# Performance work log

Measured on AMD Instinct MI355X. Metric: run time of the kernel, lower is better.

The kernel has to match this reference:

```python
import jax, jax.numpy as jnp
import numpy as np

B, N, P, C, H = 8, 512, 16, 512, 8
HD = C // H  # 64


def setup_inputs() -> dict:
    key = jax.random.key(0)
    k1, k2, k3, k4, k5 = jax.random.split(key, 5)
    x = jax.random.normal(k1, (B, N, P, C), dtype=jnp.float32)
    # binary observation mask; force slot 0 valid so masked mean never divides by 0
    mask = (jax.random.uniform(k2, (B, N, P)) > 0.3).astype(jnp.float32)
    mask = mask.at[:, :, 0].set(1.0)
    lens = jax.random.randint(k3, (B,), 1, N)
    lens_mask = jnp.ones((B, N), dtype=jnp.float32)
    # parameters (torch Linear stored as [in, out] here; qkv_bias=False, proj has bias)
    Wqkv = jax.random.normal(k4, (C, 3 * C), dtype=jnp.float32) * (1.0 / np.sqrt(C))
    Wproj = jax.random.normal(k5, (C, C), dtype=jnp.float32) * (1.0 / np.sqrt(C))
    bproj = jnp.zeros((C,), dtype=jnp.float32)
    return {"x": x, "mask": mask, "lens": lens, "lens_mask": lens_mask,
            "Wqkv": Wqkv, "Wproj": Wproj, "bproj": bproj}


def reference(x, mask, lens, lens_mask, Wqkv, Wproj, bproj):
    # lens / lens_mask are unused by the original forward
    b, n, p, c = x.shape
    h, hd = H, c // H
    qkv = jnp.einsum('bnpc,cd->bnpd', x, Wqkv).reshape(b, n, p, 3, h, hd)
    # q: take P-slot 0                       -> [B,H,N,hd]
    q = qkv[:, :, 0, 0].transpose(0, 2, 1, 3)
    # k: masked mean over P                  -> [B,H,N,hd]
    m = mask[..., None, None]                      # [B,N,P,1,1]
    k = (jnp.where(m > 0, qkv[:, :, :, 1], 0.0).sum(axis=2) / m.sum(axis=2))
    k = k.transpose(0, 2, 1, 3)
    # v: pack P into channel dim             -> [B,H,N,hd*P]
    v = qkv[:, :, :, 2].transpose(0, 3, 1, 4, 2).reshape(b, h, n, hd * p)
    # SDPA over N (scale by 1/sqrt(head_dim of q))
    scale = 1.0 / np.sqrt(hd)
    attn = jax.nn.softmax(jnp.einsum('bhnd,bhmd->bhnm', q, k) * scale, axis=-1)
    out = jnp.einsum('bhnm,bhme->bhne', attn, v)            # [B,H,N,hd*P]
    # unpack P back out                       -> [B,N,P,C]
    out = out.reshape(b, h, n, hd, p).transpose(0, 2, 4, 1, 3).reshape(b, n, p, c)
    return out @ Wproj + bproj
```

## Files before the change

### kernel.cpp

```cpp
#include <hip/hip_runtime.h>

typedef _Float16 f16;
typedef __attribute__((ext_vector_type(8))) _Float16 half8;
typedef __attribute__((ext_vector_type(2))) _Float16 half2v;
typedef __attribute__((ext_vector_type(4))) float float4v;

#define MODE_QK 0
#define MODE_V 1
#define MODE_PV 2
#define MODE_PROJ 3


__device__ __forceinline__ void gload16(const f16* g, f16* l) {
    __builtin_amdgcn_global_load_lds(
        (const __attribute__((address_space(1))) void*)g,
        (__attribute__((address_space(3))) void*)l, 16, 0, 0);
}

__global__ __launch_bounds__(256) void prep_kernel(
    const float* __restrict__ x, const float* __restrict__ mask,
    const float* __restrict__ Wqkv, const float* __restrict__ Wproj,
    f16* __restrict__ xf, f16* __restrict__ xmean,
    f16* __restrict__ WT, f16* __restrict__ WpT)
{
    if (blockIdx.x >= 4096) {
        int idx = (blockIdx.x - 4096) * 256 + threadIdx.x;
        if (idx < 1536 * 512) {
            int d = idx >> 9, c = idx & 511;
            WT[idx] = (f16)Wqkv[c * 1536 + d];
        } else {
            int i2 = idx - 1536 * 512;
            int d = i2 >> 9, c = i2 & 511;
            WpT[i2] = (f16)Wproj[c * 512 + d];
        }
        return;
    }
    int bn = blockIdx.x;
    int t = threadIdx.x;
    const float* xrow = x + (size_t)bn * 16 * 512;
    const float* mrow = mask + (size_t)bn * 16;
    float msum = 0.f;
    #pragma unroll
    for (int p = 0; p < 16; p++) msum += mrow[p];
    int c = t * 2;
    float a0 = 0.f, a1 = 0.f;
    #pragma unroll
    for (int p = 0; p < 16; p++) {
        float2 v = *(const float2*)(xrow + p * 512 + c);
        float m = mrow[p];
        a0 += m * v.x; a1 += m * v.y;
        half2v h; h[0] = (f16)v.x; h[1] = (f16)v.y;
        *(half2v*)(xf + (size_t)bn * 16 * 512 + p * 512 + c) = h;
    }
    float inv = 1.f / msum;
    half2v hm; hm[0] = (f16)(a0 * inv); hm[1] = (f16)(a1 * inv);
    *(half2v*)(xmean + (size_t)bn * 512 + c) = hm;
}

template<int MODE, int NXB, int NYB>
__global__ __launch_bounds__(256) void gemm128(
    const f16* __restrict__ pA, const f16* __restrict__ pA2,
    const f16* __restrict__ pB,
    f16* __restrict__ outa, f16* __restrict__ outb,
    float* __restrict__ outf, const float* __restrict__ bias)
{
    __shared__ __align__(16) f16 sm[16384];
    const int t = threadIdx.x;
    const int lane = t & 63;
    const int w = t >> 6;
    const int wm = w & 1, wn = w >> 1;
    const int quad = lane >> 4, l15 = lane & 15;

    const int chunk = (int)gridDim.x >> 3;
    const int L = ((int)blockIdx.x & 7) * chunk + ((int)blockIdx.x >> 3);
    const int xb = L & ((1 << NXB) - 1);
    const int rest = L >> NXB;
    const int yb = rest & ((1 << NYB) - 1);
    const int z = rest >> NYB;
    const int n0 = xb * 128;
    const int m0 = yb * 128;
    int vb = 0, vp = 0;

    const f16* Abase; size_t sA;
    const f16* Bbase; size_t sB;
    if constexpr (MODE == MODE_QK) {
        if (n0 < 512) { Abase = pA;  sA = 8192; }
        else          { Abase = pA2; sA = 512;  }
        Bbase = pB; sB = 512;
    } else if constexpr (MODE == MODE_V) {
        vb = z >> 4; vp = z & 15;
        Abase = pA; sA = 512;
        Bbase = pB + ((size_t)vb * 512 * 16 + vp) * 512; sB = 8192;
    } else if constexpr (MODE == MODE_PV) {
        Abase = pA + (size_t)z * 512 * 512; sA = 512;
        Bbase = pB + (size_t)z * 1024 * 512; sB = 512;
    } else {
        Abase = pA; sA = 512;
        Bbase = pB; sB = 512;
    }

    const int rlo = (lane >> 2);
    const int kof = (((lane & 3) ^ ((rlo >> 1) & 3)) * 8);
    const f16* ga0 = Abase + (size_t)(m0 + w * 16 + rlo) * sA + kof;
    const f16* ga1 = Abase + (size_t)(m0 + (w + 4) * 16 + rlo) * sA + kof;
    const f16* gb0 = Bbase + (size_t)(n0 + w * 16 + rlo) * sB + kof;
    const f16* gb1 = Bbase + (size_t)(n0 + (w + 4) * 16 + rlo) * sB + kof;

    float4v acc[4][4];
    #pragma unroll
    for (int i = 0; i < 4; i++)
        #pragma unroll
        for (int j = 0; j < 4; j++)
            acc[i][j] = (float4v){0.f, 0.f, 0.f, 0.f};

    {
        f16* d = sm;
        gload16(ga0, d + w * 512); gload16(ga1, d + (w + 4) * 512);
        gload16(gb0, d + 4096 + w * 512); gload16(gb1, d + 4096 + (w + 4) * 512);
        ga0 += 32; ga1 += 32; gb0 += 32; gb1 += 32;
    }
    const int sws = (l15 >> 1) & 3;
    int cur = 0;
    for (int kt = 0; kt < 16; kt++) {
        __syncthreads();
        if (kt < 15) {
            f16* d = sm + (cur ^ 1) * 8192;
            gload16(ga0, d + w * 512); gload16(ga1, d + (w + 4) * 512);
            gload16(gb0, d + 4096 + w * 512); gload16(gb1, d + 4096 + (w + 4) * 512);
            ga0 += 32; ga1 += 32; gb0 += 32; gb1 += 32;
        }
        const f16* Asr = sm + cur * 8192;
        const f16* Bsr = Asr + 4096;
        half8 af[4], bf[4];
        #pragma unroll
        for (int mi = 0; mi < 4; mi++)
            af[mi] = *(const half8*)&Asr[(wm * 64 + mi * 16 + l15) * 32 +
                                         ((quad ^ sws) * 8)];
        #pragma unroll
        for (int ni = 0; ni < 4; ni++)
            bf[ni] = *(const half8*)&Bsr[(wn * 64 + ni * 16 + l15) * 32 +
                                         ((quad ^ sws) * 8)];
        #pragma unroll
        for (int mi = 0; mi < 4; mi++)
            #pragma unroll
            for (int ni = 0; ni < 4; ni++)
                acc[mi][ni] = __builtin_amdgcn_mfma_f32_16x16x32_f16(
                    af[mi], bf[ni], acc[mi][ni], 0, 0, 0);
        cur ^= 1;
    }

    __syncthreads();

    if constexpr (MODE == MODE_PROJ) {
        float* pwf = (float*)sm + w * 1088;
        const int rr4 = lane >> 4, c4c = (lane & 15) * 4;
        float4v bb = *(const float4v*)&bias[n0 + wn * 64 + c4c];
        #pragma unroll
        for (int mi = 0; mi < 4; mi++) {
            #pragma unroll
            for (int ni = 0; ni < 4; ni++)
                #pragma unroll
                for (int i = 0; i < 4; i++)
                    pwf[(quad * 4 + i) * 68 + ni * 16 + l15] = acc[mi][ni][i];
            #pragma unroll
            for (int s = 0; s < 4; s++) {
                int r = s * 4 + rr4;
                float4v v = *(const float4v*)&pwf[r * 68 + c4c];
                *(float4v*)&outf[(size_t)(m0 + wm * 64 + mi * 16 + r) * 512 +
                                 n0 + wn * 64 + c4c] = v + bb;
            }
        }
    } else {
        f16* pw = sm + w * 2304;
        const int rr8 = lane >> 3, c8 = (lane & 7) * 8;
        #pragma unroll
        for (int hf = 0; hf < 2; hf++) {
            #pragma unroll
            for (int mh = 0; mh < 2; mh++) {
                int mi = hf * 2 + mh;
                #pragma unroll
                for (int ni = 0; ni < 4; ni++)
                    #pragma unroll
                    for (int i = 0; i < 4; i++)
                        pw[(mh * 16 + quad * 4 + i) * 72 + ni * 16 + l15] =
                            (f16)acc[mi][ni][i];
            }
            #pragma unroll
            for (int s = 0; s < 4; s++) {
                int r = s * 8 + rr8;
                half8 v = *(const half8*)&pw[r * 72 + c8];
                int gr = m0 + wm * 64 + hf * 32 + r;
                int gc = n0 + wn * 64 + c8;
                if constexpr (MODE == MODE_QK) {
                    int b = gr >> 9, n = gr & 511;
                    if (gc < 512)
                        *(half8*)&outa[(((size_t)(b * 8 + (gc >> 6))) * 512 + n) * 64 + (gc & 63)] = v;
                    else {
                        int jj = gc - 512;
                        *(half8*)&outb[(((size_t)(b * 8 + (jj >> 6))) * 512 + n) * 64 + (jj & 63)] = v;
                    }
                } else if constexpr (MODE == MODE_V) {
                    int h = gr >> 6, dd = gr & 63;
                    *(half8*)&outa[(((size_t)(vb * 8 + h)) * 1024 + vp * 64 + dd) * 512 + gc] = v;
                } else {
                    int p = gc >> 6, dd = gc & 63;
                    int b = z >> 3, h = z & 7;
                    *(half8*)&outa[((size_t)(b * 512 + gr) * 16 + p) * 512 + h * 64 + dd] = v;
                }
            }
        }
    }
}

__global__ __launch_bounds__(256) void qk_softmax_kernel(
    const f16* __restrict__ q, const f16* __restrict__ k, f16* __restrict__ Pout)
{
    __shared__ __align__(16) f16 sm[16896];
    const int t = threadIdx.x;
    const int lane = t & 63, w = t >> 6;
    const int quad = lane >> 4, l15 = lane & 15;
    const int L = ((int)blockIdx.x & 7) * 64 + ((int)blockIdx.x >> 3);
    const int bh = L >> 3;
    const int n0 = (L & 7) * 64;

    const f16* kbase = k + (size_t)bh * 512 * 64;
    const f16* qp = q + ((size_t)bh * 512 + n0 + w * 16 + l15) * 64 + quad * 8;
    half8 a0 = *(const half8*)qp;
    half8 a1 = *(const half8*)(qp + 32);

    float4v acc[32];
    #pragma unroll
    for (int f = 0; f < 32; f++) acc[f] = (float4v){0.f, 0.f, 0.f, 0.f};

    const int srow = lane >> 3, scol = lane & 7;
    #pragma unroll
    for (int c = 0; c < 4; c++) {
        __syncthreads();
        #pragma unroll
        for (int i = 0; i < 4; i++) {
            int ci2 = w * 4 + i;
            int row = ci2 * 8 + srow;
            gload16(kbase + c * 8192 + row * 64 + ((scol ^ (row & 7)) << 3),
                    sm + ci2 * 512 + lane * 8);
        }
        __syncthreads();
        #pragma unroll
        for (int fl = 0; fl < 8; fl++) {
            int row16 = fl * 16 + l15;
            int sw = row16 & 7;
            half8 b0 = *(const half8*)&sm[row16 * 64 + ((quad ^ sw) << 3)];
            half8 b1 = *(const half8*)&sm[row16 * 64 + (((quad + 4) ^ sw) << 3)];
            acc[c * 8 + fl] = __builtin_amdgcn_mfma_f32_16x16x32_f16(
                a0, b0, acc[c * 8 + fl], 0, 0, 0);
            acc[c * 8 + fl] = __builtin_amdgcn_mfma_f32_16x16x32_f16(
                a1, b1, acc[c * 8 + fl], 0, 0, 0);
        }
    }

    float mx0 = -3e38f, mx1 = -3e38f, mx2 = -3e38f, mx3 = -3e38f;
    #pragma unroll
    for (int f = 0; f < 32; f++) {
        mx0 = fmaxf(mx0, acc[f][0]); mx1 = fmaxf(mx1, acc[f][1]);
        mx2 = fmaxf(mx2, acc[f][2]); mx3 = fmaxf(mx3, acc[f][3]);
    }
    #pragma unroll
    for (int off = 1; off < 16; off <<= 1) {
        mx0 = fmaxf(mx0, __shfl_xor(mx0, off));
        mx1 = fmaxf(mx1, __shfl_xor(mx1, off));
        mx2 = fmaxf(mx2, __shfl_xor(mx2, off));
        mx3 = fmaxf(mx3, __shfl_xor(mx3, off));
    }
    float s0 = 0.f, s1 = 0.f, s2 = 0.f, s3 = 0.f;
    #pragma unroll
    for (int f = 0; f < 32; f++) {
        float e0 = __expf(0.125f * (acc[f][0] - mx0));
        float e1 = __expf(0.125f * (acc[f][1] - mx1));
        float e2 = __expf(0.125f * (acc[f][2] - mx2));
        float e3 = __expf(0.125f * (acc[f][3] - mx3));
        acc[f][0] = e0; acc[f][1] = e1; acc[f][2] = e2; acc[f][3] = e3;
        s0 += e0; s1 += e1; s2 += e2; s3 += e3;
    }
    #pragma unroll
    for (int off = 1; off < 16; off <<= 1) {
        s0 += __shfl_xor(s0, off);
        s1 += __shfl_xor(s1, off);
        s2 += __shfl_xor(s2, off);
        s3 += __shfl_xor(s3, off);
    }
    float r0 = 1.f / s0, r1 = 1.f / s1, r2 = 1.f / s2, r3 = 1.f / s3;

    __syncthreads();
    f16* pb = sm + w * 4224;
    const int rr = lane >> 2, cb = (lane & 3) * 64;
    #pragma unroll
    for (int cc = 0; cc < 2; cc++) {
        #pragma unroll
        for (int ff = 0; ff < 16; ff++) {
            int f = cc * 16 + ff;
            pb[(quad * 4 + 0) * 264 + ff * 16 + l15] = (f16)(acc[f][0] * r0);
            pb[(quad * 4 + 1) * 264 + ff * 16 + l15] = (f16)(acc[f][1] * r1);
            pb[(quad * 4 + 2) * 264 + ff * 16 + l15] = (f16)(acc[f][2] * r2);
            pb[(quad * 4 + 3) * 264 + ff * 16 + l15] = (f16)(acc[f][3] * r3);
        }
        size_t gb = ((size_t)bh * 512 + n0 + w * 16 + rr) * 512 + cc * 256 + cb;
        #pragma unroll
        for (int s = 0; s < 8; s++) {
            half8 v = *(const half8*)&pb[rr * 264 + cb + s * 8];
            *(half8*)&Pout[gb + s * 8] = v;
        }
    }
}

extern "C" void kernel_launch(void* const* d_in, const int* in_sizes, int n_in,
                              void* d_out, int out_size, void* d_ws, size_t ws_size,
                              hipStream_t stream)
{
    (void)in_sizes; (void)n_in; (void)out_size; (void)ws_size;
    const float* x     = (const float*)d_in[0];
    const float* mask  = (const float*)d_in[1];
    const float* Wqkv  = (const float*)d_in[4];
    const float* Wproj = (const float*)d_in[5];
    const float* bproj = (const float*)d_in[6];
    float* out = (float*)d_out;
    char* ws = (char*)d_ws;

    f16* xf16  = (f16*)(ws + 0);
    f16* vT    = (f16*)(ws + 67108864);
    f16* xmean = (f16*)(ws + 134217728);
    f16* WT    = (f16*)(ws + 138412032);
    f16* WpT   = (f16*)(ws + 139984896);
    f16* qb    = (f16*)(ws + 140509184);
    f16* kb    = (f16*)(ws + 144703488);
    f16* Pm    = (f16*)(ws + 148897792);
    f16* ypre  = xf16;

    prep_kernel<<<dim3(8192), dim3(256), 0, stream>>>(
        x, mask, Wqkv, Wproj, xf16, xmean, WT, WpT);
    gemm128<MODE_QK, 3, 5><<<dim3(256), dim3(256), 0, stream>>>(
        xf16, xmean, WT, qb, kb, nullptr, nullptr);
    gemm128<MODE_V, 2, 2><<<dim3(2048), dim3(256), 0, stream>>>(
        WT + 1024 * 512, nullptr, xf16, vT, nullptr, nullptr, nullptr);
    qk_softmax_kernel<<<dim3(512), dim3(256), 0, stream>>>(qb, kb, Pm);
    gemm128<MODE_PV, 3, 2><<<dim3(2048), dim3(256), 0, stream>>>(
        Pm, nullptr, vT, ypre, nullptr, nullptr, nullptr);
    gemm128<MODE_PROJ, 2, 9><<<dim3(2048), dim3(256), 0, stream>>>(
        ypre, nullptr, WpT, nullptr, nullptr, out, bproj);
}
```

Baseline: 421.9 us.

## Triple-buffer GEMM K-loop and load full K tile at once in QK softmax

The shared GEMM kernel moves from double to triple buffering in LDS. It uses explicit vmcnt waits and raw barriers so two tiles are in flight while one is computed, which should hide global-to-LDS latency better. The QK softmax kernel now loads the whole 512x64 K block into LDS up front, replacing four chunked load/sync rounds with a single wait. Both kernels use more LDS (48KB and 64KB), which can lower occupancy.

```diff
diff --git a/kernel.cpp b/kernel.cpp
--- a/kernel.cpp
+++ b/kernel.cpp
@@ -64,7 +64,7 @@
     f16* __restrict__ outa, f16* __restrict__ outb,
     float* __restrict__ outf, const float* __restrict__ bias)
 {
-    __shared__ __align__(16) f16 sm[16384];
+    __shared__ __align__(16) f16 sm[24576];
     const int t = threadIdx.x;
     const int lane = t & 63;
     const int w = t >> 6;
@@ -113,41 +113,62 @@
         for (int j = 0; j < 4; j++)
             acc[i][j] = (float4v){0.f, 0.f, 0.f, 0.f};
 
-    {
-        f16* d = sm;
-        gload16(ga0, d + w * 512); gload16(ga1, d + (w + 4) * 512);
-        gload16(gb0, d + 4096 + w * 512); gload16(gb1, d + 4096 + (w + 4) * 512);
-        ga0 += 32; ga1 += 32; gb0 += 32; gb1 += 32;
-    }
     const int sws = (l15 >> 1) & 3;
-    int cur = 0;
-    for (int kt = 0; kt < 16; kt++) {
-        __syncthreads();
-        if (kt < 15) {
-            f16* d = sm + (cur ^ 1) * 8192;
-            gload16(ga0, d + w * 512); gload16(ga1, d + (w + 4) * 512);
-            gload16(gb0, d + 4096 + w * 512); gload16(gb1, d + 4096 + (w + 4) * 512);
-            ga0 += 32; ga1 += 32; gb0 += 32; gb1 += 32;
-        }
-        const f16* Asr = sm + cur * 8192;
-        const f16* Bsr = Asr + 4096;
-        half8 af[4], bf[4];
-        #pragma unroll
-        for (int mi = 0; mi < 4; mi++)
-            af[mi] = *(const half8*)&Asr[(wm * 64 + mi * 16 + l15) * 32 +
-                                         ((quad ^ sws) * 8)];
-        #pragma unroll
-        for (int ni = 0; ni < 4; ni++)
-            bf[ni] = *(const half8*)&Bsr[(wn * 64 + ni * 16 + l15) * 32 +
-                                         ((quad ^ sws) * 8)];
-        #pragma unroll
-        for (int mi = 0; mi < 4; mi++)
-            #pragma unroll
-            for (int ni = 0; ni < 4; ni++)
-                acc[mi][ni] = __builtin_amdgcn_mfma_f32_16x16x32_f16(
-                    af[mi], bf[ni], acc[mi][ni], 0, 0, 0);
-        cur ^= 1;
-    }
+
+#define STAGE(dst)                                                     \
+    do {                                                               \
+        f16* d_ = (dst);                                               \
+        gload16(ga0, d_ + w * 512); gload16(ga1, d_ + (w + 4) * 512);  \
+        gload16(gb0, d_ + 4096 + w * 512);                             \
+        gload16(gb1, d_ + 4096 + (w + 4) * 512);                       \
+        ga0 += 32; ga1 += 32; gb0 += 32; gb1 += 32;                    \
+    } while (0)
+
+#define COMPUTE(buf)                                                         \
+    do {                                                                     \
+        const f16* Asr_ = (buf);                                             \
+        const f16* Bsr_ = Asr_ + 4096;                                       \
+        half8 af[4], bf[4];                                                  \
+        _Pragma("unroll")                                                    \
+        for (int mi = 0; mi < 4; mi++)                                       \
+            af[mi] = *(const half8*)&Asr_[(wm * 64 + mi * 16 + l15) * 32 +   \
+                                          ((quad ^ sws) * 8)];               \
+        _Pragma("unroll")                                                    \
+        for (int ni = 0; ni < 4; ni++)                                       \
+            bf[ni] = *(const half8*)&Bsr_[(wn * 64 + ni * 16 + l15) * 32 +   \
+                                          ((quad ^ sws) * 8)];               \
+        _Pragma("unroll")                                                    \
+        for (int mi = 0; mi < 4; mi++)                                       \
+            _Pragma("unroll")                                                \
+            for (int ni = 0; ni < 4; ni++)                                   \
+                acc[mi][ni] = __builtin_amdgcn_mfma_f32_16x16x32_f16(        \
+                    af[mi], bf[ni], acc[mi][ni], 0, 0, 0);                   \
+    } while (0)
+
+    f16* pc = sm;
+    f16* pn = sm + 8192;
+    f16* pf = sm + 16384;
+    STAGE(pc);
+    STAGE(pn);
+    for (int kt = 0; kt < 14; kt++) {
+        asm volatile("s_waitcnt vmcnt(4)" ::: "memory");
+        __builtin_amdgcn_s_barrier();
+        __builtin_amdgcn_sched_barrier(0);
+        STAGE(pf);
+        COMPUTE(pc);
+        f16* tmp = pc; pc = pn; pn = pf; pf = tmp;
+    }
+    asm volatile("s_waitcnt vmcnt(4)" ::: "memory");
+    __builtin_amdgcn_s_barrier();
+    __builtin_amdgcn_sched_barrier(0);
+    COMPUTE(pc);
+    { f16* tmp = pc; pc = pn; pn = pf; pf = tmp; }
+    asm volatile("s_waitcnt vmcnt(0)" ::: "memory");
+    __builtin_amdgcn_s_barrier();
+    __builtin_amdgcn_sched_barrier(0);
+    COMPUTE(pc);
+#undef STAGE
+#undef COMPUTE
 
     __syncthreads();
 
@@ -215,7 +236,7 @@
 __global__ __launch_bounds__(256) void qk_softmax_kernel(
     const f16* __restrict__ q, const f16* __restrict__ k, f16* __restrict__ Pout)
 {
-    __shared__ __align__(16) f16 sm[16896];
+    __shared__ __align__(16) f16 sm[32768];
     const int t = threadIdx.x;
     const int lane = t & 63, w = t >> 6;
     const int quad = lane >> 4, l15 = lane & 15;
@@ -224,37 +245,33 @@
     const int n0 = (L & 7) * 64;
 
     const f16* kbase = k + (size_t)bh * 512 * 64;
+
+    #pragma unroll
+    for (int i = 0; i < 16; i++) {
+        int cid = i * 256 + t;
+        int row = cid >> 3, off = cid & 7;
+        gload16(kbase + row * 64 + ((off ^ (row & 7)) << 3),
+                sm + i * 2048 + w * 512 + (lane & 63) * 8);
+    }
     const f16* qp = q + ((size_t)bh * 512 + n0 + w * 16 + l15) * 64 + quad * 8;
     half8 a0 = *(const half8*)qp;
     half8 a1 = *(const half8*)(qp + 32);
 
+    asm volatile("s_waitcnt vmcnt(0)" ::: "memory");
+    __builtin_amdgcn_s_barrier();
+    __builtin_amdgcn_sched_barrier(0);
+
     float4v acc[32];
     #pragma unroll
     for (int f = 0; f < 32; f++) acc[f] = (float4v){0.f, 0.f, 0.f, 0.f};
-
-    const int srow = lane >> 3, scol = lane & 7;
-    #pragma unroll
-    for (int c = 0; c < 4; c++) {
-        __syncthreads();
-        #pragma unroll
-        for (int i = 0; i < 4; i++) {
-            int ci2 = w * 4 + i;
-            int row = ci2 * 8 + srow;
-            gload16(kbase + c * 8192 + row * 64 + ((scol ^ (row & 7)) << 3),
-                    sm + ci2 * 512 + lane * 8);
-        }
-        __syncthreads();
-        #pragma unroll
-        for (int fl = 0; fl < 8; fl++) {
-            int row16 = fl * 16 + l15;
-            int sw = row16 & 7;
-            half8 b0 = *(const half8*)&sm[row16 * 64 + ((quad ^ sw) << 3)];
-            half8 b1 = *(const half8*)&sm[row16 * 64 + (((quad + 4) ^ sw) << 3)];
-            acc[c * 8 + fl] = __builtin_amdgcn_mfma_f32_16x16x32_f16(
-                a0, b0, acc[c * 8 + fl], 0, 0, 0);
-            acc[c * 8 + fl] = __builtin_amdgcn_mfma_f32_16x16x32_f16(
-                a1, b1, acc[c * 8 + fl], 0, 0, 0);
-        }
+    #pragma unroll
+    for (int fl = 0; fl < 32; fl++) {
+        int row16 = fl * 16 + l15;
+        int sw = row16 & 7;
+        half8 b0 = *(const half8*)&sm[row16 * 64 + ((quad ^ sw) << 3)];
+        half8 b1 = *(const half8*)&sm[row16 * 64 + (((quad + 4) ^ sw) << 3)];
+        acc[fl] = __builtin_amdgcn_mfma_f32_16x16x32_f16(a0, b0, acc[fl], 0, 0, 0);
+        acc[fl] = __builtin_amdgcn_mfma_f32_16x16x32_f16(a1, b1, acc[fl], 0, 0, 0);
     }
 
     float mx0 = -3e38f, mx1 = -3e38f, mx2 = -3e38f, mx3 = -3e38f;
```

Result: faster. 405.3 us (-3.9%).
